# Performance work log

Measured on AMD Instinct MI355X. Metric: run time of the kernel, lower is better.

Reference implementation:

```python
import jax, jax.numpy as jnp
import numpy as np


def setup_inputs() -> dict:
    key = jax.random.key(0)
    ks = jax.random.split(key, 5)
    B, P_LEN, D = 16, 1024, 512
    scale = 0.02
    return {
        "P": jax.random.normal(ks[0], (B, P_LEN, D), dtype=jnp.float32),
        "w_atten": jax.random.normal(ks[1], (3 * D,), dtype=jnp.float32) * scale,
        "w1": jax.random.normal(ks[2], (2 * D, D), dtype=jnp.float32) * scale,
        "w2": jax.random.normal(ks[3], (2 * D, D), dtype=jnp.float32) * scale,
        "w3": jax.random.normal(ks[4], (2 * D, D), dtype=jnp.float32) * scale,
        "b1": jnp.zeros((D,), dtype=jnp.float32),
        "b2": jnp.zeros((D,), dtype=jnp.float32),
        "b3": jnp.zeros((D,), dtype=jnp.float32),
    }


def reference(P, w_atten, w1, w2, w3, b1, b2, b3):
    # P: (b, p, d). Original builds a (b, p, 3d, p) concat tensor; the score
    # A[b,i,j] = wa . P_i + wb . P_j + wc . (P_i * P_j) factorizes exactly:
    d = P.shape[-1]
    wa, wb, wc = w_atten[:d], w_atten[d:2 * d], w_atten[2 * d:]
    si = P @ wa                                   # (b, p)  contribution of row token i
    sj = P @ wb                                   # (b, p)  contribution of col token j
    A = si[:, :, None] + sj[:, None, :] + jnp.einsum("bid,bjd->bij", P * wc, P)
    SA = jax.nn.softmax(A, axis=2)                # softmax over j
    attn_res = jnp.einsum("bij,bjd->bid", SA, P)  # (b, p, d)
    # Fuse gate (DecayingDropout is identity at inference)
    Pc = jnp.concatenate([P, attn_res], axis=2)   # (b, p, 2d)
    z = jnp.tanh(Pc @ w1 + b1)
    r = jax.nn.sigmoid(Pc @ w2 + b2)
    f = jax.nn.sigmoid(Pc @ w3 + b3)
    return r * P + f * z
```

## Files before the change

### kernel.cpp

```cpp
#include <hip/hip_runtime.h>
#include <stdint.h>

#define S_LEN 1024
#define DDIM  512
#define NBATCH 16

typedef __attribute__((ext_vector_type(8))) short bf16x8;
typedef __attribute__((ext_vector_type(4))) float f32x4;
typedef unsigned short ushort_t;

__device__ __forceinline__ unsigned short f2bf(float x) {
  union { float f; uint32_t u; } v; v.f = x;
  return (unsigned short)((v.u + 0x7fffu + ((v.u >> 16) & 1u)) >> 16);
}
__device__ __forceinline__ float bf2f(unsigned short h) {
  union { float f; uint32_t u; } v; v.u = ((uint32_t)h) << 16;
  return v.f;
}

#define GL16(g, l) __builtin_amdgcn_global_load_lds(                          \
    (const __attribute__((address_space(1))) void*)(g),                       \
    (__attribute__((address_space(3))) void*)(l), 16, 0, 0)

__global__ __launch_bounds__(256) void prep_rows(
    const float* __restrict__ P, const float* __restrict__ w_atten,
    unsigned short* __restrict__ Pbf, unsigned short* __restrict__ Qbf,
    float* __restrict__ sj) {
  int wave = threadIdx.x >> 6, lane = threadIdx.x & 63;
  int row = blockIdx.x * 4 + wave;
  const float* prow = P + (size_t)row * DDIM;
  float s = 0.f;
#pragma unroll
  for (int h = 0; h < 2; ++h) {
    int d = h * 256 + lane * 4;
    float4 p  = *(const float4*)(prow + d);
    float4 wb = *(const float4*)(w_atten + DDIM + d);
    float4 wc = *(const float4*)(w_atten + 2 * DDIM + d);
    s += p.x * wb.x + p.y * wb.y + p.z * wb.z + p.w * wb.w;
    ushort4 pb, qb;
    pb.x = f2bf(p.x); pb.y = f2bf(p.y); pb.z = f2bf(p.z); pb.w = f2bf(p.w);
    qb.x = f2bf(p.x * wc.x); qb.y = f2bf(p.y * wc.y);
    qb.z = f2bf(p.z * wc.z); qb.w = f2bf(p.w * wc.w);
    *(ushort4*)(Pbf + (size_t)row * DDIM + d) = pb;
    *(ushort4*)(Qbf + (size_t)row * DDIM + d) = qb;
  }
#pragma unroll
  for (int o = 32; o; o >>= 1) s += __shfl_xor(s, o);
  if (lane == 0) sj[row] = s;
}

__global__ __launch_bounds__(256) void transpose_f2b(
    const float* __restrict__ in, unsigned short* __restrict__ out,
    int R, int C, long inStride, long outStride) {
  __shared__ unsigned short T[64][65];
  in  += (size_t)blockIdx.z * inStride;
  out += (size_t)blockIdx.z * outStride;
  int c0 = blockIdx.x * 64, r0 = blockIdx.y * 64;
  int tx = threadIdx.x & 63, ty = threadIdx.x >> 6;
#pragma unroll
  for (int rr = 0; rr < 16; ++rr) {
    int rl = ty * 16 + rr;
    T[rl][tx] = f2bf(in[(size_t)(r0 + rl) * C + c0 + tx]);
  }
  __syncthreads();
#pragma unroll
  for (int rr = 0; rr < 16; ++rr) {
    int cl = ty * 16 + rr;
    out[(size_t)(c0 + cl) * R + r0 + tx] = T[tx][cl];
  }
}

#define GSTEP(KT)                                                             \
  if constexpr ((KT) < NT) {                                                  \
    if constexpr ((KT) + 2 < NT) {                                            \
      ushort_t* dA_ = lA[((KT) + 2) % 3];                                     \
      ushort_t* dB_ = lB[((KT) + 2) % 3];                                     \
      if constexpr ((KT) + 2 < KS32) {                                        \
        GL16(aLo0 + ((KT) + 2) * 32, dA_ + lbase);                            \
        GL16(aLo1 + ((KT) + 2) * 32, dA_ + 2048 + lbase);                     \
      } else {                                                                \
        GL16(aHi0 + ((KT) + 2 - KS32) * 32, dA_ + lbase);                     \
        GL16(aHi1 + ((KT) + 2 - KS32) * 32, dA_ + 2048 + lbase);              \
      }                                                                       \
      GL16(bB0 + ((KT) + 2) * 32, dB_ + lbase);                               \
      GL16(bB1 + ((KT) + 2) * 32, dB_ + 2048 + lbase);                        \
    }                                                                         \
    {                                                                         \
      const ushort_t* Ard_ = lA[(KT) % 3];                                    \
      const ushort_t* Brd_ = lB[(KT) % 3];                                    \
      bf16x8 af[4], bfr[4];                                                   \
      _Pragma("unroll") for (int m = 0; m < 4; ++m)                           \
        af[m] = *(const bf16x8*)(Ard_ + (wr * 64 + m * 16 + frow) * 32 + fswz); \
      _Pragma("unroll") for (int n = 0; n < 4; ++n)                           \
        bfr[n] = *(const bf16x8*)(Brd_ + (wc * 64 + n * 16 + frow) * 32 + fswz); \
      __builtin_amdgcn_s_setprio(1);                                          \
      _Pragma("unroll") for (int m = 0; m < 4; ++m)                           \
      _Pragma("unroll") for (int n = 0; n < 4; ++n)                           \
        acc[m][n] = __builtin_amdgcn_mfma_f32_16x16x32_bf16(af[m], bfr[n],    \
                                                            acc[m][n], 0, 0, 0); \
      __builtin_amdgcn_s_setprio(0);                                          \
    }                                                                         \
    if constexpr ((KT) + 1 < NT) {                                            \
      if constexpr ((KT) + 2 < NT)                                            \
        asm volatile("s_waitcnt vmcnt(4) lgkmcnt(0)" ::: "memory");           \
      else                                                                    \
        asm volatile("s_waitcnt vmcnt(0) lgkmcnt(0)" ::: "memory");           \
      __builtin_amdgcn_s_barrier();                                           \
    }                                                                         \
  }

template<int NT, int KS32, int EPI>
__global__ __launch_bounds__(256) void gemm_tb(
    const ushort_t* __restrict__ A,
    const ushort_t* __restrict__ A2,
    const ushort_t* __restrict__ Bt,
    ushort_t* __restrict__ C,
    const float* __restrict__ bias,
    const float* __restrict__ bias2,
    const float* __restrict__ bias3,
    int N, int K, int lda,
    long sAb, long sBb, long sCb, long sBiasb) {
  __shared__ __align__(16) ushort_t lA[3][4096];
  __shared__ __align__(16) ushort_t lB[3][4096];
  const int t = threadIdx.x, lane = t & 63, wave = t >> 6;

  const int gx = gridDim.x, gy = gridDim.y;
  int hblk = blockIdx.x + gx * (blockIdx.y + gy * blockIdx.z);
  int cpx = (gx * gy * (int)gridDim.z) >> 3;
  int wk = (hblk & 7) * cpx + (hblk >> 3);
  const int bx = wk % gx; int rem = wk / gx;
  const int by = rem % gy;
  const int z  = rem / gy;

  A += (size_t)z * sAb;
  A2 += (size_t)z * sAb;
  Bt += (size_t)z * sBb;
  C += (size_t)z * sCb;
  if (bias) bias += (size_t)z * sBiasb;
  const int bm = by * 128, bn = bx * 128;

  f32x4 acc[4][4];
#pragma unroll
  for (int m = 0; m < 4; ++m)
#pragma unroll
    for (int n = 0; n < 4; ++n) acc[m][n] = {0.f, 0.f, 0.f, 0.f};

  const int wr = wave >> 1, wc = wave & 1;
  const int frow = lane & 15;
  const int fswz = (((lane >> 4) ^ ((frow >> 1) & 3)) * 8);
  const int srow = t >> 2;
  const int skc = (((t & 3) ^ ((t >> 3) & 3)) * 8);
  const int lbase = (t & 192) * 8;

  const ushort_t* aLo0 = A + (size_t)(bm + srow) * lda + skc;
  const ushort_t* aLo1 = aLo0 + (size_t)64 * lda;
  const ushort_t* aHi0 = A2 + (size_t)(bm + srow) * lda + skc;
  const ushort_t* aHi1 = aHi0 + (size_t)64 * lda;
  const ushort_t* bB0  = Bt + (size_t)(bn + srow) * K + skc;
  const ushort_t* bB1  = bB0 + (size_t)64 * K;

  GL16(aLo0,      lA[0] + lbase);   GL16(aLo1,      lA[0] + 2048 + lbase);
  GL16(bB0,       lB[0] + lbase);   GL16(bB1,       lB[0] + 2048 + lbase);
  GL16(aLo0 + 32, lA[1] + lbase);   GL16(aLo1 + 32, lA[1] + 2048 + lbase);
  GL16(bB0 + 32,  lB[1] + lbase);   GL16(bB1 + 32,  lB[1] + 2048 + lbase);
  asm volatile("s_waitcnt vmcnt(4)" ::: "memory");
  __builtin_amdgcn_s_barrier();

  GSTEP(0)  GSTEP(1)  GSTEP(2)  GSTEP(3)  GSTEP(4)  GSTEP(5)  GSTEP(6)  GSTEP(7)
  GSTEP(8)  GSTEP(9)  GSTEP(10) GSTEP(11) GSTEP(12) GSTEP(13) GSTEP(14) GSTEP(15)
  GSTEP(16) GSTEP(17) GSTEP(18) GSTEP(19) GSTEP(20) GSTEP(21) GSTEP(22) GSTEP(23)
  GSTEP(24) GSTEP(25) GSTEP(26) GSTEP(27) GSTEP(28) GSTEP(29) GSTEP(30) GSTEP(31)

  const int seg = bn >> 9;
  const float* bp = bias;
  if (EPI == 4) bp = (seg == 0) ? bias : ((seg == 1) ? bias2 : bias3);
#pragma unroll
  for (int m = 0; m < 4; ++m) {
    int row0 = bm + wr * 64 + m * 16 + (lane >> 4) * 4;
#pragma unroll
    for (int n = 0; n < 4; ++n) {
      int col = bn + wc * 64 + n * 16 + frow;
      float bc = (EPI >= 1) ? bp[(EPI == 4) ? (col & 511) : col] : 0.f;
#pragma unroll
      for (int i = 0; i < 4; ++i) {
        float v = acc[m][n][i];
        if (EPI == 1) v += bc;
        if (EPI == 4) {
          v += bc;
          v = (seg == 0) ? tanhf(v) : 1.f / (1.f + __expf(-v));
        }
        C[(size_t)(row0 + i) * N + col] = f2bf(v);
      }
    }
  }
}

__global__ __launch_bounds__(256) void softmax_rows(unsigned short* __restrict__ Sb) {
  __shared__ float red[8];
  unsigned short* p = Sb + (size_t)blockIdx.x * S_LEN;
  int t = threadIdx.x, wave = t >> 6, lane = t & 63;
  ushort4 u = *(ushort4*)(p + t * 4);
  float v0 = bf2f(u.x), v1 = bf2f(u.y), v2 = bf2f(u.z), v3 = bf2f(u.w);
  float mx = fmaxf(fmaxf(v0, v1), fmaxf(v2, v3));
#pragma unroll
  for (int o = 32; o; o >>= 1) mx = fmaxf(mx, __shfl_xor(mx, o));
  if (lane == 0) red[wave] = mx;
  __syncthreads();
  mx = fmaxf(fmaxf(red[0], red[1]), fmaxf(red[2], red[3]));
  float e0 = __expf(v0 - mx), e1 = __expf(v1 - mx);
  float e2 = __expf(v2 - mx), e3 = __expf(v3 - mx);
  float ss = e0 + e1 + e2 + e3;
#pragma unroll
  for (int o = 32; o; o >>= 1) ss += __shfl_xor(ss, o);
  if (lane == 0) red[4 + wave] = ss;
  __syncthreads();
  float inv = 1.f / (red[4] + red[5] + red[6] + red[7]);
  u.x = f2bf(e0 * inv); u.y = f2bf(e1 * inv);
  u.z = f2bf(e2 * inv); u.w = f2bf(e3 * inv);
  *(ushort4*)(p + t * 4) = u;
}

__global__ __launch_bounds__(256) void final_out(
    const float* __restrict__ P, const unsigned short* __restrict__ Cm,
    float* __restrict__ out) {
  size_t i = ((size_t)blockIdx.x * 256 + threadIdx.x) * 4;
  size_t row = i >> 9;
  int col = (int)(i & 511);
  const unsigned short* base = Cm + row * 1536 + col;
  ushort4 z4 = *(const ushort4*)(base);
  ushort4 r4 = *(const ushort4*)(base + 512);
  ushort4 f4 = *(const ushort4*)(base + 1024);
  float4 p = *(const float4*)(P + i);
  float4 o;
  o.x = bf2f(r4.x) * p.x + bf2f(f4.x) * bf2f(z4.x);
  o.y = bf2f(r4.y) * p.y + bf2f(f4.y) * bf2f(z4.y);
  o.z = bf2f(r4.z) * p.z + bf2f(f4.z) * bf2f(z4.z);
  o.w = bf2f(r4.w) * p.w + bf2f(f4.w) * bf2f(z4.w);
  *(float4*)(out + i) = o;
}

extern "C" void kernel_launch(void* const* d_in, const int* in_sizes, int n_in,
                              void* d_out, int out_size, void* d_ws, size_t ws_size,
                              hipStream_t stream) {
  const float* P  = (const float*)d_in[0];
  const float* wa = (const float*)d_in[1];
  const float* w1 = (const float*)d_in[2];
  const float* w2 = (const float*)d_in[3];
  const float* w3 = (const float*)d_in[4];
  const float* b1 = (const float*)d_in[5];
  const float* b2 = (const float*)d_in[6];
  const float* b3 = (const float*)d_in[7];
  float* out = (float*)d_out;
  char* ws = (char*)d_ws;
  const size_t MB = 1024 * 1024;

  unsigned short* Pbf  = (unsigned short*)(ws + 0);
  unsigned short* PT   = (unsigned short*)(ws + 16 * MB);
  unsigned short* Qbf  = (unsigned short*)(ws + 32 * MB);
  unsigned short* Sbuf = (unsigned short*)(ws + 48 * MB);
  unsigned short* attn = (unsigned short*)(ws + 80 * MB);
  unsigned short* Wt   = (unsigned short*)(ws + 96 * MB);
  float*          sj   = (float*)(ws + 99 * MB);
  unsigned short* Cmlp = (unsigned short*)(ws + 16 * MB);

  const long SD = (long)S_LEN * DDIM;
  const long SS = (long)S_LEN * S_LEN;

  prep_rows<<<4096, 256, 0, stream>>>(P, wa, Pbf, Qbf, sj);
  transpose_f2b<<<dim3(8, 16, NBATCH), 256, 0, stream>>>(P, PT, S_LEN, DDIM, SD, SD);
  transpose_f2b<<<dim3(8, 16, 1), 256, 0, stream>>>(w1, Wt,          1024, 512, 0, 0);
  transpose_f2b<<<dim3(8, 16, 1), 256, 0, stream>>>(w2, Wt + SD,     1024, 512, 0, 0);
  transpose_f2b<<<dim3(8, 16, 1), 256, 0, stream>>>(w3, Wt + 2 * SD, 1024, 512, 0, 0);

  gemm_tb<16, 999, 1><<<dim3(8, 8, NBATCH), 256, 0, stream>>>(
      Qbf, Qbf, Pbf, Sbuf, sj, nullptr, nullptr,
      1024, 512, 512, SD, SD, SS, S_LEN);
  softmax_rows<<<16384, 256, 0, stream>>>(Sbuf);
  gemm_tb<32, 999, 0><<<dim3(4, 8, NBATCH), 256, 0, stream>>>(
      Sbuf, Sbuf, PT, attn, nullptr, nullptr, nullptr,
      512, 1024, 1024, SS, SD, SD, 0);
  gemm_tb<32, 16, 4><<<dim3(12, 128, 1), 256, 0, stream>>>(
      Pbf, attn, Wt, Cmlp, b1, b2, b3,
      1536, 1024, 512, 0, 0, 0, 0);

  final_out<<<8192, 256, 0, stream>>>(P, Cmlp, out);
}
```

Baseline: 196.9 us.

## Fuse gate GEMM with final elementwise output and transpose from bf16 copy

Replaces the 1536-wide gate GEMM plus separate final_out kernel with one mlp_fused kernel. Each block computes the z, r and f columns for the same 64 output columns together and applies tanh/sigmoid and r*P+f*z directly. This removes the bf16 intermediate write and reread and one launch. It also transposes P from the already converted bf16 buffer instead of the fp32 input, which halves that read. The fused kernel uses a 2-stage double buffer with __syncthreads instead of the 3-stage pipeline, which may expose more load latency.

```diff
diff --git a/kernel.cpp b/kernel.cpp
--- a/kernel.cpp
+++ b/kernel.cpp
@@ -70,18 +70,34 @@
   }
 }
 
+__global__ __launch_bounds__(256) void transpose_b2b(
+    const unsigned short* __restrict__ in, unsigned short* __restrict__ out,
+    int R, int C, long inStride, long outStride) {
+  __shared__ unsigned short T[64][65];
+  in  += (size_t)blockIdx.z * inStride;
+  out += (size_t)blockIdx.z * outStride;
+  int c0 = blockIdx.x * 64, r0 = blockIdx.y * 64;
+  int tx = threadIdx.x & 63, ty = threadIdx.x >> 6;
+#pragma unroll
+  for (int rr = 0; rr < 16; ++rr) {
+    int rl = ty * 16 + rr;
+    T[rl][tx] = in[(size_t)(r0 + rl) * C + c0 + tx];
+  }
+  __syncthreads();
+#pragma unroll
+  for (int rr = 0; rr < 16; ++rr) {
+    int cl = ty * 16 + rr;
+    out[(size_t)(c0 + cl) * R + r0 + tx] = T[tx][cl];
+  }
+}
+
 #define GSTEP(KT)                                                             \
   if constexpr ((KT) < NT) {                                                  \
     if constexpr ((KT) + 2 < NT) {                                            \
       ushort_t* dA_ = lA[((KT) + 2) % 3];                                     \
       ushort_t* dB_ = lB[((KT) + 2) % 3];                                     \
-      if constexpr ((KT) + 2 < KS32) {                                        \
-        GL16(aLo0 + ((KT) + 2) * 32, dA_ + lbase);                            \
-        GL16(aLo1 + ((KT) + 2) * 32, dA_ + 2048 + lbase);                     \
-      } else {                                                                \
-        GL16(aHi0 + ((KT) + 2 - KS32) * 32, dA_ + lbase);                     \
-        GL16(aHi1 + ((KT) + 2 - KS32) * 32, dA_ + 2048 + lbase);              \
-      }                                                                       \
+      GL16(aLo0 + ((KT) + 2) * 32, dA_ + lbase);                              \
+      GL16(aLo1 + ((KT) + 2) * 32, dA_ + 2048 + lbase);                       \
       GL16(bB0 + ((KT) + 2) * 32, dB_ + lbase);                               \
       GL16(bB1 + ((KT) + 2) * 32, dB_ + 2048 + lbase);                        \
     }                                                                         \
@@ -109,15 +125,12 @@
     }                                                                         \
   }
 
-template<int NT, int KS32, int EPI>
+template<int NT, int EPI>
 __global__ __launch_bounds__(256) void gemm_tb(
     const ushort_t* __restrict__ A,
-    const ushort_t* __restrict__ A2,
     const ushort_t* __restrict__ Bt,
     ushort_t* __restrict__ C,
     const float* __restrict__ bias,
-    const float* __restrict__ bias2,
-    const float* __restrict__ bias3,
     int N, int K, int lda,
     long sAb, long sBb, long sCb, long sBiasb) {
   __shared__ __align__(16) ushort_t lA[3][4096];
@@ -133,7 +146,6 @@
   const int z  = rem / gy;
 
   A += (size_t)z * sAb;
-  A2 += (size_t)z * sAb;
   Bt += (size_t)z * sBb;
   C += (size_t)z * sCb;
   if (bias) bias += (size_t)z * sBiasb;
@@ -154,8 +166,6 @@
 
   const ushort_t* aLo0 = A + (size_t)(bm + srow) * lda + skc;
   const ushort_t* aLo1 = aLo0 + (size_t)64 * lda;
-  const ushort_t* aHi0 = A2 + (size_t)(bm + srow) * lda + skc;
-  const ushort_t* aHi1 = aHi0 + (size_t)64 * lda;
   const ushort_t* bB0  = Bt + (size_t)(bn + srow) * K + skc;
   const ushort_t* bB1  = bB0 + (size_t)64 * K;
 
@@ -171,25 +181,129 @@
   GSTEP(16) GSTEP(17) GSTEP(18) GSTEP(19) GSTEP(20) GSTEP(21) GSTEP(22) GSTEP(23)
   GSTEP(24) GSTEP(25) GSTEP(26) GSTEP(27) GSTEP(28) GSTEP(29) GSTEP(30) GSTEP(31)
 
-  const int seg = bn >> 9;
-  const float* bp = bias;
-  if (EPI == 4) bp = (seg == 0) ? bias : ((seg == 1) ? bias2 : bias3);
 #pragma unroll
   for (int m = 0; m < 4; ++m) {
     int row0 = bm + wr * 64 + m * 16 + (lane >> 4) * 4;
 #pragma unroll
     for (int n = 0; n < 4; ++n) {
       int col = bn + wc * 64 + n * 16 + frow;
-      float bc = (EPI >= 1) ? bp[(EPI == 4) ? (col & 511) : col] : 0.f;
+      float bc = (EPI >= 1) ? bias[col] : 0.f;
 #pragma unroll
       for (int i = 0; i < 4; ++i) {
         float v = acc[m][n][i];
         if (EPI == 1) v += bc;
-        if (EPI == 4) {
-          v += bc;
-          v = (seg == 0) ? tanhf(v) : 1.f / (1.f + __expf(-v));
-        }
         C[(size_t)(row0 + i) * N + col] = f2bf(v);
+      }
+    }
+  }
+}
+
+#define MSTEP(KT)                                                             \
+  {                                                                           \
+    if ((KT) + 1 < 32) {                                                      \
+      ushort_t* dA_ = lA[((KT) + 1) & 1];                                     \
+      ushort_t* dB_ = lB[((KT) + 1) & 1];                                     \
+      if ((KT) + 1 < 16) {                                                    \
+        GL16(aLo0 + ((KT) + 1) * 32, dA_ + lbase);                            \
+        GL16(aLo1 + ((KT) + 1) * 32, dA_ + 2048 + lbase);                     \
+      } else {                                                                \
+        GL16(aHi0 + ((KT) + 1 - 16) * 32, dA_ + lbase);                       \
+        GL16(aHi1 + ((KT) + 1 - 16) * 32, dA_ + 2048 + lbase);                \
+      }                                                                       \
+      GL16(bS0 + ((KT) + 1) * 32, dB_ + lbase);                               \
+      GL16(bS1 + ((KT) + 1) * 32, dB_ + 2048 + lbase);                        \
+      GL16(bS2 + ((KT) + 1) * 32, dB_ + 4096 + lbase);                        \
+    }                                                                         \
+    {                                                                         \
+      const ushort_t* Ard_ = lA[(KT) & 1];                                    \
+      const ushort_t* Brd_ = lB[(KT) & 1];                                    \
+      bf16x8 af[4];                                                           \
+      _Pragma("unroll") for (int m = 0; m < 4; ++m)                           \
+        af[m] = *(const bf16x8*)(Ard_ + (wr * 64 + m * 16 + frow) * 32 + fswz); \
+      _Pragma("unroll") for (int s = 0; s < 3; ++s) {                         \
+        bf16x8 b0 = *(const bf16x8*)(Brd_ + s * 2048 +                        \
+                                     (wc * 32 + frow) * 32 + fswz);           \
+        bf16x8 b1v = *(const bf16x8*)(Brd_ + s * 2048 +                       \
+                                      (wc * 32 + 16 + frow) * 32 + fswz);     \
+        __builtin_amdgcn_s_setprio(1);                                        \
+        _Pragma("unroll") for (int m = 0; m < 4; ++m) {                       \
+          acc[s][m][0] = __builtin_amdgcn_mfma_f32_16x16x32_bf16(             \
+              af[m], b0, acc[s][m][0], 0, 0, 0);                              \
+          acc[s][m][1] = __builtin_amdgcn_mfma_f32_16x16x32_bf16(             \
+              af[m], b1v, acc[s][m][1], 0, 0, 0);                             \
+        }                                                                     \
+        __builtin_amdgcn_s_setprio(0);                                        \
+      }                                                                       \
+    }                                                                         \
+    if ((KT) < 31) __syncthreads();                                           \
+  }
+
+__global__ __launch_bounds__(256, 2) void mlp_fused(
+    const ushort_t* __restrict__ Pbf,
+    const ushort_t* __restrict__ attn,
+    const ushort_t* __restrict__ Wt,
+    const float* __restrict__ P,
+    const float* __restrict__ b1,
+    const float* __restrict__ b2,
+    const float* __restrict__ b3,
+    float* __restrict__ out) {
+  __shared__ __align__(16) ushort_t lA[2][4096];
+  __shared__ __align__(16) ushort_t lB[2][3 * 2048];
+  const int t = threadIdx.x, lane = t & 63, wave = t >> 6;
+
+  int hblk = blockIdx.x + 8 * blockIdx.y;
+  int wk = (hblk & 7) * 128 + (hblk >> 3);
+  const int bx = wk & 7;
+  const int by = wk >> 3;
+  const int bm = by * 128, bn = bx * 64;
+
+  f32x4 acc[3][4][2];
+#pragma unroll
+  for (int s = 0; s < 3; ++s)
+#pragma unroll
+    for (int m = 0; m < 4; ++m)
+#pragma unroll
+      for (int n = 0; n < 2; ++n) acc[s][m][n] = {0.f, 0.f, 0.f, 0.f};
+
+  const int wr = wave >> 1, wc = wave & 1;
+  const int frow = lane & 15;
+  const int fswz = (((lane >> 4) ^ ((frow >> 1) & 3)) * 8);
+  const int srow = t >> 2;
+  const int skc = (((t & 3) ^ ((t >> 3) & 3)) * 8);
+  const int lbase = (t & 192) * 8;
+
+  const ushort_t* aLo0 = Pbf + (size_t)(bm + srow) * 512 + skc;
+  const ushort_t* aLo1 = aLo0 + (size_t)64 * 512;
+  const ushort_t* aHi0 = attn + (size_t)(bm + srow) * 512 + skc;
+  const ushort_t* aHi1 = aHi0 + (size_t)64 * 512;
+  const ushort_t* bS0 = Wt + (size_t)(bn + srow) * 1024 + skc;
+  const ushort_t* bS1 = bS0 + (size_t)512 * 1024;
+  const ushort_t* bS2 = bS0 + (size_t)1024 * 1024;
+
+  GL16(aLo0, lA[0] + lbase);  GL16(aLo1, lA[0] + 2048 + lbase);
+  GL16(bS0,  lB[0] + lbase);  GL16(bS1,  lB[0] + 2048 + lbase);
+  GL16(bS2,  lB[0] + 4096 + lbase);
+  __syncthreads();
+
+  MSTEP(0)  MSTEP(1)  MSTEP(2)  MSTEP(3)  MSTEP(4)  MSTEP(5)  MSTEP(6)  MSTEP(7)
+  MSTEP(8)  MSTEP(9)  MSTEP(10) MSTEP(11) MSTEP(12) MSTEP(13) MSTEP(14) MSTEP(15)
+  MSTEP(16) MSTEP(17) MSTEP(18) MSTEP(19) MSTEP(20) MSTEP(21) MSTEP(22) MSTEP(23)
+  MSTEP(24) MSTEP(25) MSTEP(26) MSTEP(27) MSTEP(28) MSTEP(29) MSTEP(30) MSTEP(31)
+
+#pragma unroll
+  for (int m = 0; m < 4; ++m) {
+    int row0 = bm + wr * 64 + m * 16 + (lane >> 4) * 4;
+#pragma unroll
+    for (int n = 0; n < 2; ++n) {
+      int col = bn + wc * 32 + n * 16 + frow;
+      float B1 = b1[col], B2 = b2[col], B3 = b3[col];
+#pragma unroll
+      for (int i = 0; i < 4; ++i) {
+        size_t idx = (size_t)(row0 + i) * 512 + col;
+        float z = tanhf(acc[0][m][n][i] + B1);
+        float r = 1.f / (1.f + __expf(-(acc[1][m][n][i] + B2)));
+        float f = 1.f / (1.f + __expf(-(acc[2][m][n][i] + B3)));
+        out[idx] = r * P[idx] + f * z;
       }
     }
   }
@@ -218,25 +332,6 @@
   u.x = f2bf(e0 * inv); u.y = f2bf(e1 * inv);
   u.z = f2bf(e2 * inv); u.w = f2bf(e3 * inv);
   *(ushort4*)(p + t * 4) = u;
-}
-
-__global__ __launch_bounds__(256) void final_out(
-    const float* __restrict__ P, const unsigned short* __restrict__ Cm,
-    float* __restrict__ out) {
-  size_t i = ((size_t)blockIdx.x * 256 + threadIdx.x) * 4;
-  size_t row = i >> 9;
-  int col = (int)(i & 511);
-  const unsigned short* base = Cm + row * 1536 + col;
-  ushort4 z4 = *(const ushort4*)(base);
-  ushort4 r4 = *(const ushort4*)(base + 512);
-  ushort4 f4 = *(const ushort4*)(base + 1024);
-  float4 p = *(const float4*)(P + i);
-  float4 o;
-  o.x = bf2f(r4.x) * p.x + bf2f(f4.x) * bf2f(z4.x);
-  o.y = bf2f(r4.y) * p.y + bf2f(f4.y) * bf2f(z4.y);
-  o.z = bf2f(r4.z) * p.z + bf2f(f4.z) * bf2f(z4.z);
-  o.w = bf2f(r4.w) * p.w + bf2f(f4.w) * bf2f(z4.w);
-  *(float4*)(out + i) = o;
 }
 
 extern "C" void kernel_launch(void* const* d_in, const int* in_sizes, int n_in,
@@ -261,27 +356,21 @@
   unsigned short* attn = (unsigned short*)(ws + 80 * MB);
   unsigned short* Wt   = (unsigned short*)(ws + 96 * MB);
   float*          sj   = (float*)(ws + 99 * MB);
-  unsigned short* Cmlp = (unsigned short*)(ws + 16 * MB);
 
   const long SD = (long)S_LEN * DDIM;
   const long SS = (long)S_LEN * S_LEN;
 
   prep_rows<<<4096, 256, 0, stream>>>(P, wa, Pbf, Qbf, sj);
-  transpose_f2b<<<dim3(8, 16, NBATCH), 256, 0, stream>>>(P, PT, S_LEN, DDIM, SD, SD);
+  transpose_b2b<<<dim3(8, 16, NBATCH), 256, 0, stream>>>(Pbf, PT, S_LEN, DDIM, SD, SD);
   transpose_f2b<<<dim3(8, 16, 1), 256, 0, stream>>>(w1, Wt,          1024, 512, 0, 0);
   transpose_f2b<<<dim3(8, 16, 1), 256, 0, stream>>>(w2, Wt + SD,     1024, 512, 0, 0);
   transpose_f2b<<<dim3(8, 16, 1), 256, 0, stream>>>(w3, Wt + 2 * SD, 1024, 512, 0, 0);
 
-  gemm_tb<16, 999, 1><<<dim3(8, 8, NBATCH), 256, 0, stream>>>(
-      Qbf, Qbf, Pbf, Sbuf, sj, nullptr, nullptr,
-      1024, 512, 512, SD, SD, SS, S_LEN);
+  gemm_tb<16, 1><<<dim3(8, 8, NBATCH), 256, 0, stream>>>(
+      Qbf, Pbf, Sbuf, sj, 1024, 512, 512, SD, SD, SS, S_LEN);
   softmax_rows<<<16384, 256, 0, stream>>>(Sbuf);
-  gemm_tb<32, 999, 0><<<dim3(4, 8, NBATCH), 256, 0, stream>>>(
-      Sbuf, Sbuf, PT, attn, nullptr, nullptr, nullptr,
-      512, 1024, 1024, SS, SD, SD, 0);
-  gemm_tb<32, 16, 4><<<dim3(12, 128, 1), 256, 0, stream>>>(
-      Pbf, attn, Wt, Cmlp, b1, b2, b3,
-      1536, 1024, 512, 0, 0, 0, 0);
-
-  final_out<<<8192, 256, 0, stream>>>(P, Cmlp, out);
-}
+  gemm_tb<32, 0><<<dim3(4, 8, NBATCH), 256, 0, stream>>>(
+      Sbuf, PT, attn, nullptr, 512, 1024, 1024, SS, SD, SD, 0);
+  mlp_fused<<<dim3(8, 128), 256, 0, stream>>>(
+      Pbf, attn, Wt, P, b1, b2, b3, out);
+}
```

Result: faster. 177.2 us (-10.0%).
